# Kernel optimization log

Measured on AMD Instinct MI355X. Metric: run time of the kernel, lower is better.

The kernel has to match this reference:

```python
import jax, jax.numpy as jnp
import numpy as np

# ---- static config (mirrors CE defaults) ----
PS = 7        # patch size
WS = 27       # search window (per side)
S0 = 4        # query stride (stride0)
KS = 100      # k_s: top-k kept by search
KA = 100      # k_a: top-k used for aggregation
SCALE = 10.0  # softmax_scale
CI = 16       # inter_channels


def conv2d(x, w, b, pad):
    y = jax.lax.conv_general_dilated(
        x, w, (1, 1), [(pad, pad), (pad, pad)],
        dimension_numbers=("NCHW", "OIHW", "NCHW"))
    return y + b[None, :, None, None]


def all_patches(v):
    """[T,C,H,W] -> [T, H*W, C*PS*PS]; top-left anchored PSxPS patches,
    edge-clamped at the border (dnls-style bounded patch extraction)."""
    t, c, h, w = v.shape
    ii = jnp.clip(jnp.arange(h)[:, None] + jnp.arange(PS)[None, :], 0, h - 1)
    jj = jnp.clip(jnp.arange(w)[:, None] + jnp.arange(PS)[None, :], 0, w - 1)
    p = v[:, :, ii][:, :, :, :, jj]          # [T,C,H,PS,W,PS]
    p = p.transpose(0, 2, 4, 1, 3, 5)        # [T,H,W,C,PS,PS]
    return p.reshape(t, h * w, c * PS * PS)


def setup_inputs():
    key = jax.random.key(0)
    ks = jax.random.split(key, 4)
    vid = jax.random.normal(ks[0], (4, 64, 128, 128), jnp.float32)
    g_w = jax.random.normal(ks[1], (CI, 64, 3, 3), jnp.float32) * 0.05
    g_b = jnp.zeros((CI,), jnp.float32)
    theta_w = jax.random.normal(ks[2], (CI, 64, 1, 1), jnp.float32) * 0.1
    theta_b = jnp.zeros((CI,), jnp.float32)
    return {"vid": vid, "g_w": g_w, "g_b": g_b,
            "theta_w": theta_w, "theta_b": theta_b}


def reference(vid, g_w, g_b, theta_w, theta_b):
    t, c, h, w = vid.shape
    nH, nW = h // S0, w // S0
    Q, N = nH * nW, h * w

    # feature extraction (g -> search features, theta -> aggregation values)
    v1 = conv2d(vid, g_w, g_b, 1)          # [T,CI,H,W]
    v2 = conv2d(vid, theta_w, theta_b, 0)  # [T,CI,H,W]

    # windowed k-NN patch search: query grid (stride0) vs all keys (stride1=1)
    P1 = all_patches(v1)                                    # [T,N,D]
    qis = jnp.arange(nH) * S0
    qjs = jnp.arange(nW) * S0
    qflat = (qis[:, None] * w + qjs[None, :]).reshape(-1)   # [Q]
    Pq = P1[:, qflat]                                       # [T,Q,D]
    scores = jnp.einsum("tqd,tnd->tqn", Pq, P1)             # [T,Q,N]

    off = jnp.arange(WS) - WS // 2
    ci = jnp.clip(qis[:, None] + off, 0, h - 1)             # [nH,WS]
    cj = jnp.clip(qjs[:, None] + off, 0, w - 1)             # [nW,WS]
    cand = (ci[:, None, :, None] * w + cj[None, :, None, :]).reshape(Q, WS * WS)
    dists = jnp.take_along_axis(scores, cand[None], axis=2)  # [T,Q,WS*WS]

    d_k, widx = jax.lax.top_k(dists, KS)                    # [T,Q,KS]
    inds = jnp.take_along_axis(jnp.broadcast_to(cand[None], dists.shape),
                               widx, axis=2)                # flat key positions

    # top-k softmax aggregation weights
    wgt = jax.nn.softmax(d_k[..., :KA] * SCALE, axis=-1)    # [T,Q,KA]
    inds_a = inds[..., :KA]

    # wpsum: weighted sum of value patches gathered at neighbor indices,
    # expressed as sparse-scatter matrix @ dense patch matrix
    A = jnp.zeros((t, Q, N), scores.dtype).at[
        jnp.arange(t)[:, None, None],
        jnp.arange(Q)[None, :, None],
        inds_a].add(wgt)                                    # [T,Q,N]
    P2 = all_patches(v2)                                    # [T,N,D]
    z = jnp.einsum("tqn,tnd->tqd", A, P2)                   # [T,Q,CI*PS*PS]

    # ifold: scatter-add overlapping patches + count normalization
    z = z.reshape(t, Q, CI, PS, PS).transpose(0, 2, 1, 3, 4)
    z = z.reshape(t, CI, Q * PS * PS)
    ri = jnp.clip(qis[:, None] + jnp.arange(PS), 0, h - 1)  # [nH,PS]
    rj = jnp.clip(qjs[:, None] + jnp.arange(PS), 0, w - 1)  # [nW,PS]
    pix = (ri[:, None, :, None] * w + rj[None, :, None, :]).reshape(-1)
    Y = jnp.zeros((t, CI, N), z.dtype).at[:, :, pix].add(z)
    Zc = jnp.zeros((N,), z.dtype).at[pix].add(1.0)
    y = (Y / Zc).reshape(t, CI, h, w)
    return y
```

## Files before the change

kernel.cpp:

```cpp
#include <hip/hip_runtime.h>
#include <hip/hip_bf16.h>

#define T_ 4
#define C_ 64
#define H_ 128
#define W_ 128
#define CI_ 16
#define PS_ 7
#define NC_ 729
#define S0_ 4
#define KS_ 100
#define NQ_ 1024
#define SCALE_ 10.0f
#define HW_ (H_*W_)
#define RW_ 45
#define LCAP_ 768
#define CB_ 8

typedef float v2f __attribute__((ext_vector_type(2)));
#if __has_builtin(__builtin_elementwise_fma)
#define VFMA(a, b, c) __builtin_elementwise_fma((a), (b), (c))
#else
#define VFMA(a, b, c) ((a) * (b) + (c))
#endif

__device__ __forceinline__ float4 colfix(float4 r, bool loB, bool hiB) {
  float4 o;
  o.x = loB ? 0.f : (hiB ? r.y : r.x);
  o.y = loB ? r.x : (hiB ? r.z : r.y);
  o.z = loB ? r.y : (hiB ? r.w : r.z);
  o.w = loB ? r.z : (hiB ? 0.f : r.w);
  return o;
}

__global__ __launch_bounds__(128, 1) void conv3x3_kernel(
    const float* __restrict__ vid, const float* __restrict__ gw,
    const float* __restrict__ gb, float4* __restrict__ v1cs) {
  __shared__ float wls[C_ * 9 * 4];
  const int tid = threadIdx.x;
  const int g = blockIdx.y, t = blockIdx.z;
  for (int m = tid; m < C_ * 9 * 4; m += 128) {
    int co = m & 3, ck = m >> 2;
    wls[m] = gw[((size_t)(g * 4 + co) * C_) * 9 + ck];
  }
  __syncthreads();
  const int ti0 = (blockIdx.x >> 3) * 16, tj0 = (blockIdx.x & 7) * 16;
  const int u = tid >> 3, v = tid & 7;
  const int i = ti0 + u, j0 = tj0 + 2 * v;
  const int c0 = j0 - 1;
  const int c0c = min(max(c0, 0), W_ - 4);
  const bool loB = (c0 < 0), hiB = (c0 > W_ - 4);
  const int rm1 = max(i - 1, 0), rp1 = min(i + 1, H_ - 1);
  const float mk0 = (i > 0) ? 1.f : 0.f;
  const float mk2 = (i < H_ - 1) ? 1.f : 0.f;
  const int o0 = rm1 * W_ + c0c, o1 = i * W_ + c0c, o2 = rp1 * W_ + c0c;

  float accA[4], accB[4];
#pragma unroll
  for (int co = 0; co < 4; ++co) { accA[co] = gb[g * 4 + co]; accB[co] = gb[g * 4 + co]; }

  const float* vb = vid + ((size_t)t * C_) * HW_;
#pragma unroll 1
  for (int cb = 0; cb < C_; cb += CB_) {
    float4 r[CB_][3];
#pragma unroll
    for (int c = 0; c < CB_; ++c) {
      const float* p = vb + (size_t)(cb + c) * HW_;
      r[c][0] = *(const float4*)(p + o0);
      r[c][1] = *(const float4*)(p + o1);
      r[c][2] = *(const float4*)(p + o2);
    }
#pragma unroll
    for (int c = 0; c < CB_; ++c) {
      float4 f0 = colfix(r[c][0], loB, hiB);
      float4 f1 = colfix(r[c][1], loB, hiB);
      float4 f2 = colfix(r[c][2], loB, hiB);
      f0.x *= mk0; f0.y *= mk0; f0.z *= mk0; f0.w *= mk0;
      f2.x *= mk2; f2.y *= mk2; f2.z *= mk2; f2.w *= mk2;
      const float* wc = &wls[(cb + c) * 36];
      float e0[4] = {f0.x, f0.y, f0.z, f0.w};
      float e1[4] = {f1.x, f1.y, f1.z, f1.w};
      float e2[4] = {f2.x, f2.y, f2.z, f2.w};
#pragma unroll
      for (int kj = 0; kj < 3; ++kj) {
#pragma unroll
        for (int co = 0; co < 4; ++co) {
          accA[co] = fmaf(wc[(0 * 3 + kj) * 4 + co], e0[kj],     accA[co]);
          accB[co] = fmaf(wc[(0 * 3 + kj) * 4 + co], e0[kj + 1], accB[co]);
          accA[co] = fmaf(wc[(1 * 3 + kj) * 4 + co], e1[kj],     accA[co]);
          accB[co] = fmaf(wc[(1 * 3 + kj) * 4 + co], e1[kj + 1], accB[co]);
          accA[co] = fmaf(wc[(2 * 3 + kj) * 4 + co], e2[kj],     accA[co]);
          accB[co] = fmaf(wc[(2 * 3 + kj) * 4 + co], e2[kj + 1], accB[co]);
        }
      }
    }
  }
  const size_t o = ((size_t)g * T_ + t) * HW_ + i * W_ + j0;
  v1cs[o]     = make_float4(accA[0], accA[1], accA[2], accA[3]);
  v1cs[o + 1] = make_float4(accB[0], accB[1], accB[2], accB[3]);
}

__global__ __launch_bounds__(256, 1) void conv1x1_kernel(
    const float* __restrict__ vid, const float* __restrict__ tw,
    const float* __restrict__ tb, float4* __restrict__ v2cs) {
  __shared__ float w[C_ * 4];
  const int t = blockIdx.y, cc = blockIdx.z;
  for (int m = threadIdx.x; m < C_ * 4; m += 256) {
    int o = m & 3, c = m >> 2;
    w[m] = tw[(cc * 4 + o) * C_ + c];
  }
  __syncthreads();
  const int pix = blockIdx.x * 256 + threadIdx.x;
  float acc[4];
#pragma unroll
  for (int o = 0; o < 4; ++o) acc[o] = tb[cc * 4 + o];
  const float* vb = vid + ((size_t)t * C_) * HW_ + pix;
#pragma unroll 1
  for (int c0 = 0; c0 < C_; c0 += 16) {
    float x[16];
#pragma unroll
    for (int uu = 0; uu < 16; ++uu) x[uu] = vb[(size_t)(c0 + uu) * HW_];
#pragma unroll
    for (int uu = 0; uu < 16; ++uu)
#pragma unroll
      for (int o = 0; o < 4; ++o)
        acc[o] = fmaf(w[(c0 + uu) * 4 + o], x[uu], acc[o]);
  }
  v2cs[((size_t)cc * T_ + t) * HW_ + pix] = make_float4(acc[0], acc[1], acc[2], acc[3]);
}

__global__ __launch_bounds__(512, 2) void dist_kernel(
    const float4* __restrict__ v1cs, float* __restrict__ distG,
    float* __restrict__ distB, int nch) {
  __shared__ float4 Rs[2][2048];
  const int tid = threadIdx.x;
  const int t = blockIdx.y;
  const int half = blockIdx.z;
  const int cbase = half * 2;
  const int qi0 = (blockIdx.x >> 3) * 16, qj0 = (blockIdx.x & 7) * 16;
  const int w = tid >> 6, lane = tid & 63;
  const int pr = w >> 2, dj = (w & 3) * 4;
  const int rbase = 8 * pr;
  const int qi_p = qi0 + rbase;
  const int qj = qj0 + dj;
  const int la = lane >> 1, bg = lane & 1;
  const int b_lo = max(13 - qj, 0);
  const int bs = bg ? 13 : b_lo;
  const int a_lo0 = max(13 - qi_p, 0);
  const int a_lo1 = max(9 - qi_p, 0);
  const bool compute_ok = (la < 31);

  int soff[4];
#pragma unroll
  for (int k = 0; k < 4; ++k) {
    int p = min(tid + 512 * k, RW_ * RW_ - 1);
    int uu = p / RW_, vv = p - uu * RW_;
    int row = min(max(qi0 - 13 + uu, 0), H_ - 1);
    int col = min(max(qj0 - 13 + vv, 0), W_ - 1);
    soff[k] = row * W_ + col;
  }

  v2f acc0[14], acc1[14];
#pragma unroll
  for (int j = 0; j < 14; ++j) { acc0[j] = (v2f){0.f, 0.f}; acc1[j] = (v2f){0.f, 0.f}; }

  float4 st[4];
  {
    const float4* src = v1cs + ((size_t)cbase * T_ + t) * HW_;
#pragma unroll
    for (int k = 0; k < 4; ++k) st[k] = src[soff[k]];
  }
  int cur = 0;
#pragma unroll 1
  for (int ci = 0; ci < nch; ++ci) {
    float4* buf = &Rs[cur][0];
#pragma unroll
    for (int k = 0; k < 4; ++k) buf[tid + 512 * k] = st[k];
    if (ci + 1 < nch) {
      const float4* src = v1cs + ((size_t)(cbase + ci + 1) * T_ + t) * HW_;
#pragma unroll
      for (int k = 0; k < 4; ++k) st[k] = src[soff[k]];
    }
    __syncthreads();
    if (compute_ok) {
#pragma unroll 1
      for (int r = 0; r < 7; ++r) {
        v2f q0lo[7], q0hi[7], q1lo[7], q1hi[7];
        const float4* q0row = &buf[(rbase + 13 + r) * RW_ + dj + 13];
#pragma unroll
        for (int s = 0; s < 7; ++s) {
          float4 qq = q0row[s];
          q0lo[s] = (v2f){qq.x, qq.y};
          q0hi[s] = (v2f){qq.z, qq.w};
          float4 q2 = q0row[4 * RW_ + s];
          q1lo[s] = (v2f){q2.x, q2.y};
          q1hi[s] = (v2f){q2.z, q2.w};
        }
        const float4* crow = &buf[(rbase + la + r) * RW_ + dj + bs];
#pragma unroll
        for (int y = 0; y < 20; ++y) {
          float4 vv4 = crow[y];
          v2f vlo = (v2f){vv4.x, vv4.y}, vhi = (v2f){vv4.z, vv4.w};
          const int s_lo = (y > 13) ? (y - 13) : 0;
          const int s_hi = (y < 6) ? y : 6;
#pragma unroll
          for (int s = s_lo; s <= s_hi; ++s) {
            int j = y - s;
            acc0[j] = VFMA(q0lo[s], vlo, acc0[j]);
            acc0[j] = VFMA(q0hi[s], vhi, acc0[j]);
            acc1[j] = VFMA(q1lo[s], vlo, acc1[j]);
            acc1[j] = VFMA(q1hi[s], vhi, acc1[j]);
          }
        }
      }
    }
    cur ^= 1;
  }
  if (compute_ok) {
    float* outB = half ? distB : distG;
    const int q0q = ((qi_p >> 2) << 5) + (qj >> 2);
    if (la >= a_lo0 && la <= 26) {
      float* out = outB + ((size_t)t * NQ_ + q0q) * NC_ + la * 27 + bs;
#pragma unroll
      for (int j = 0; j < 14; ++j) out[j] = acc0[j].x + acc0[j].y;
    }
    const int a1 = la - 4;
    if (a1 >= a_lo1 && a1 <= 26) {
      float* out = outB + ((size_t)t * NQ_ + (q0q + 32)) * NC_ + a1 * 27 + bs;
#pragma unroll
      for (int j = 0; j < 14; ++j) out[j] = acc1[j].x + acc1[j].y;
    }
  }
}

__global__ __launch_bounds__(256) void select_kernel(
    const float* __restrict__ distA, const float* __restrict__ distB, int dual,
    int* __restrict__ sel_n, float* __restrict__ sel_w,
    float* __restrict__ wsum_out) {
  __shared__ float dist[NC_];
  __shared__ unsigned int ukey[NC_];
  __shared__ float redf[4];
  __shared__ unsigned int hist[256];
  __shared__ int lk[LCAP_];
  __shared__ unsigned int lkey[LCAP_];
  __shared__ unsigned int scal[6];

  const int tid = threadIdx.x;
  const int lane = tid & 63, wid = tid >> 6;
  const int q = blockIdx.x, t = blockIdx.y;
  const int qi = (q >> 5) * S0_, qj = (q & 31) * S0_;
  const int a_lo = max(13 - qi, 0), b_lo = max(13 - qj, 0);
  const size_t base = ((size_t)t * NQ_ + q) * NC_;

  for (int h = tid; h < 256; h += 256) hist[h] = 0;
  if (tid == 0) { scal[2] = 0; scal[3] = 0; }
  float lmax = -INFINITY;
  for (int k = tid; k < NC_; k += 256) {
    int aa = k / 27, bb = k - aa * 27;
    int kk = max(aa, a_lo) * 27 + max(bb, b_lo);
    float d = distA[base + kk];
    if (dual) d += distB[base + kk];
    dist[k] = d;
    unsigned int u = __float_as_uint(d);
    ukey[k] = u ^ (((unsigned int)((int)u >> 31)) | 0x80000000u);
    lmax = fmaxf(lmax, d);
  }
#pragma unroll
  for (int off = 32; off > 0; off >>= 1)
    lmax = fmaxf(lmax, __shfl_down(lmax, off, 64));
  if (lane == 0) redf[wid] = lmax;
  __syncthreads();
  const float dmax = fmaxf(fmaxf(redf[0], redf[1]), fmaxf(redf[2], redf[3]));
  for (int k = tid; k < NC_; k += 256) atomicAdd(&hist[ukey[k] >> 24], 1u);
  __syncthreads();
  if (wid == 0) {
    int s4 = (int)(hist[lane * 4] + hist[lane * 4 + 1] + hist[lane * 4 + 2] + hist[lane * 4 + 3]);
    int s = s4;
#pragma unroll
    for (int off = 1; off < 64; off <<= 1) {
      int o = __shfl_down(s, off, 64);
      if (lane + off < 64) s += o;
    }
    int above = s - s4;
    if (above < KS_ && s >= KS_) {
      int run = above;
#pragma unroll
      for (int bb = 3; bb >= 0; --bb) {
        int h = (int)hist[lane * 4 + bb];
        if (run + h >= KS_) { scal[0] = (unsigned int)(lane * 4 + bb); scal[1] = (unsigned int)run; break; }
        run += h;
      }
    }
  }
  __syncthreads();
  const unsigned int beta = scal[0];
  const int run = (int)scal[1];
  for (int h = tid; h < 256; h += 256) hist[h] = 0;
  __syncthreads();
  for (int k = tid; k < NC_; k += 256)
    if ((ukey[k] >> 24) == beta) atomicAdd(&hist[(ukey[k] >> 16) & 0xFFu], 1u);
  __syncthreads();
  if (wid == 0) {
    int s4 = (int)(hist[lane * 4] + hist[lane * 4 + 1] + hist[lane * 4 + 2] + hist[lane * 4 + 3]);
    int s = s4;
#pragma unroll
    for (int off = 1; off < 64; off <<= 1) {
      int o = __shfl_down(s, off, 64);
      if (lane + off < 64) s += o;
    }
    int above = run + s - s4;
    if (above < KS_ && run + s >= KS_) {
      int r2 = above;
#pragma unroll
      for (int bb = 3; bb >= 0; --bb) {
        int h = (int)hist[lane * 4 + bb];
        if (r2 + h >= KS_) { scal[4] = (unsigned int)(lane * 4 + bb); scal[5] = (unsigned int)r2; break; }
        r2 += h;
      }
    }
  }
  __syncthreads();
  const unsigned int beta2 = scal[4];
  const int run2 = (int)scal[5];
  const size_t outb = ((size_t)t * NQ_ + q) * KS_;
  float lsum = 0.f;
  for (int k = tid; k < NC_; k += 256) {
    unsigned int key = ukey[k];
    unsigned int bin = key >> 24;
    bool sel = false, bdry = false;
    if (bin > beta) sel = true;
    else if (bin == beta) {
      unsigned int b2 = (key >> 16) & 0xFFu;
      if (b2 > beta2) sel = true;
      else if (b2 == beta2) bdry = true;
    }
    if (sel) {
      unsigned int slot = atomicAdd(&scal[2], 1u);
      int aa = k / 27, bb = k - aa * 27;
      int ni = min(max(qi + aa - 13, 0), H_ - 1);
      int nj = min(max(qj + bb - 13, 0), W_ - 1);
      float wv = __expf(SCALE_ * (dist[k] - dmax));
      sel_n[outb + slot] = (ni << 7) | nj;
      sel_w[outb + slot] = wv;
      lsum += wv;
    } else if (bdry) {
      unsigned int pos = atomicAdd(&scal[3], 1u);
      if (pos < LCAP_) { lk[pos] = k; lkey[pos] = key; }
    }
  }
  __syncthreads();
  const int L = min((int)scal[3], LCAP_);
  for (int i = tid; i < L; i += 256) {
    unsigned int key = lkey[i];
    int k = lk[i];
    int cnt = run2;
    for (int m = 0; m < L; ++m)
      cnt += (int)((lkey[m] > key) || (lkey[m] == key && lk[m] < k));
    if (cnt < KS_) {
      unsigned int slot = atomicAdd(&scal[2], 1u);
      int aa = k / 27, bb = k - aa * 27;
      int ni = min(max(qi + aa - 13, 0), H_ - 1);
      int nj = min(max(qj + bb - 13, 0), W_ - 1);
      float wv = __expf(SCALE_ * (dist[k] - dmax));
      sel_n[outb + slot] = (ni << 7) | nj;
      sel_w[outb + slot] = wv;
      lsum += wv;
    }
  }
#pragma unroll
  for (int off = 32; off > 0; off >>= 1) lsum += __shfl_down(lsum, off, 64);
  __syncthreads();
  if (lane == 0) redf[wid] = lsum;
  __syncthreads();
  if (tid == 0) wsum_out[t * NQ_ + q] = (redf[0] + redf[1]) + (redf[2] + redf[3]);
}

__global__ __launch_bounds__(1024) void agg_kernel(
    const float4* __restrict__ v2cs, const int* __restrict__ sel_n,
    const float* __restrict__ sel_w, const float* __restrict__ wsum,
    float* __restrict__ Y) {
  __shared__ float4 Rs[RW_ * RW_];
  __shared__ int s_off[16][KS_];
  __shared__ float s_w[16][KS_];
  const int tid = threadIdx.x;
  const int t = blockIdx.y;
  const int qi0 = (blockIdx.x >> 3) * 16, qj0 = (blockIdx.x & 7) * 16;
  const int w = tid >> 6, lane = tid & 63;
  const int di = (w >> 2) * 4, dj = (w & 3) * 4;
  const int qi = qi0 + di, qj = qj0 + dj;
  const int q = ((qi >> 2) << 5) + (qj >> 2);
  const size_t base = ((size_t)t * NQ_ + q) * KS_;
  const float inv = 1.0f / wsum[t * NQ_ + q];
  for (int k = lane; k < KS_; k += 64) {
    int n = sel_n[base + k];
    int ni = n >> 7, nj = n & 127;
    s_off[w][k] = (ni - qi0 + 13) * RW_ + (nj - qj0 + 13);
    s_w[w][k] = sel_w[base + k] * inv;
  }
  const int r = lane / 7, s = lane - r * 7;
  const int myo = r * RW_ + s;
  const int oi = min(qi + r, H_ - 1), oj = min(qj + s, W_ - 1);
#pragma unroll 1
  for (int cc = 0; cc < 4; ++cc) {
    __syncthreads();
    const float4* src = v2cs + ((size_t)cc * T_ + t) * HW_;
    for (int p = tid; p < RW_ * RW_; p += 1024) {
      int uu = p / RW_, vv = p - uu * RW_;
      int row = min(max(qi0 - 13 + uu, 0), H_ - 1);
      int col = min(max(qj0 - 13 + vv, 0), W_ - 1);
      Rs[p] = src[row * W_ + col];
    }
    __syncthreads();
    if (lane < 49) {
      float4 acc = make_float4(0.f, 0.f, 0.f, 0.f);
#pragma unroll 4
      for (int k = 0; k < KS_; ++k) {
        float wv = s_w[w][k];
        float4 v = Rs[s_off[w][k] + myo];
        acc.x = fmaf(wv, v.x, acc.x);
        acc.y = fmaf(wv, v.y, acc.y);
        acc.z = fmaf(wv, v.z, acc.z);
        acc.w = fmaf(wv, v.w, acc.w);
      }
      float* yb = Y + (((size_t)t * CI_ + cc * 4) * H_ + oi) * W_ + oj;
      atomicAdd(yb, acc.x);
      atomicAdd(yb + HW_, acc.y);
      atomicAdd(yb + 2 * HW_, acc.z);
      atomicAdd(yb + 3 * HW_, acc.w);
    }
  }
}

__device__ __forceinline__ int cov_axis(int x) {
  int c = 0;
#pragma unroll
  for (int r = 0; r < 7; ++r) {
    if (x < H_ - 1) {
      int qb = x - r;
      c += (qb >= 0 && (qb & 3) == 0) ? 1 : 0;
    } else {
      c += (r >= 3) ? 1 : 0;
    }
  }
  return c;
}

__global__ void norm_kernel(float* __restrict__ Y) {
  int idx = blockIdx.x * blockDim.x + threadIdx.x;
  if (idx >= T_ * CI_ * HW_) return;
  int p = idx & (HW_ - 1);
  float z = (float)(cov_axis(p >> 7) * cov_axis(p & 127));
  Y[idx] /= z;
}

extern "C" void kernel_launch(void* const* d_in, const int* in_sizes, int n_in,
                              void* d_out, int out_size, void* d_ws, size_t ws_size,
                              hipStream_t stream) {
  const float* vid     = (const float*)d_in[0];
  const float* g_w     = (const float*)d_in[1];
  const float* g_b     = (const float*)d_in[2];
  const float* theta_w = (const float*)d_in[3];
  const float* theta_b = (const float*)d_in[4];
  float* Y = (float*)d_out;

  float* v1cs  = (float*)d_ws;
  float* v2cs  = v1cs + (size_t)4 * T_ * HW_ * 4;
  float* distG = v2cs + (size_t)4 * T_ * HW_ * 4;
  int*   sel_n = (int*)(distG + (size_t)T_ * NQ_ * NC_);
  float* sel_w = (float*)(sel_n + (size_t)T_ * NQ_ * KS_);
  float* wsumv = sel_w + (size_t)T_ * NQ_ * KS_;
  float* distB = wsumv + (size_t)T_ * NQ_;

  const size_t need_dual =
      ((size_t)4 * T_ * HW_ * 4 * 2 + (size_t)T_ * NQ_ * NC_ * 2 +
       (size_t)T_ * NQ_ * KS_ * 2 + (size_t)T_ * NQ_) * sizeof(float);
  const int dual = (ws_size >= need_dual) ? 1 : 0;

  hipMemsetAsync(Y, 0, (size_t)out_size * sizeof(float), stream);

  conv3x3_kernel<<<dim3(64, 4, T_), 128, 0, stream>>>(vid, g_w, g_b, (float4*)v1cs);
  conv1x1_kernel<<<dim3(HW_ / 256, T_, 4), 256, 0, stream>>>(vid, theta_w, theta_b, (float4*)v2cs);
  dist_kernel<<<dim3(64, T_, dual ? 2 : 1), 512, 0, stream>>>(
      (const float4*)v1cs, distG, distB, dual ? 2 : 4);
  select_kernel<<<dim3(NQ_, T_), 256, 0, stream>>>(distG, distB, dual, sel_n, sel_w, wsumv);
  agg_kernel<<<dim3(64, T_), 1024, 0, stream>>>((const float4*)v2cs, sel_n, sel_w, wsumv, Y);
  norm_kernel<<<(T_ * CI_ * HW_ + 255) / 256, 256, 0, stream>>>(Y);
}
```

Measured before the change: 266.6 us.

## Split dist kernel work by patch rows instead of channel halves, sharing loaded tiles

The distance kernel previously split the four feature-channel groups across two grid z-slices, each loading its own halo tiles. Now one 1024-thread block loads all four channel groups once, and two 8-wave sets each compute a subset of patch rows (0-3 and 4-6) into separate partial buffers. The select kernel sums these partials as before. A fallback path uses atomics into a zeroed buffer when workspace is small. This halves global tile loads and grid size but adds an extra barrier per channel and an uneven row split (4 vs 3) between the wave sets.

```diff
diff --git a/kernel.cpp b/kernel.cpp
--- a/kernel.cpp
+++ b/kernel.cpp
@@ -129,17 +129,17 @@
   v2cs[((size_t)cc * T_ + t) * HW_ + pix] = make_float4(acc[0], acc[1], acc[2], acc[3]);
 }
 
-__global__ __launch_bounds__(512, 2) void dist_kernel(
+__global__ __launch_bounds__(1024, 4) void dist_kernel(
     const float4* __restrict__ v1cs, float* __restrict__ distG,
-    float* __restrict__ distB, int nch) {
-  __shared__ float4 Rs[2][2048];
+    float* __restrict__ distB, int use_atomic) {
+  __shared__ float4 Rs[2][2025];
   const int tid = threadIdx.x;
   const int t = blockIdx.y;
-  const int half = blockIdx.z;
-  const int cbase = half * 2;
   const int qi0 = (blockIdx.x >> 3) * 16, qj0 = (blockIdx.x & 7) * 16;
   const int w = tid >> 6, lane = tid & 63;
-  const int pr = w >> 2, dj = (w & 3) * 4;
+  const int ws = w & 7, rset = w >> 3;
+  const int r0 = rset ? 4 : 0, r1 = rset ? 7 : 4;
+  const int pr = ws >> 2, dj = (ws & 3) * 4;
   const int rbase = 8 * pr;
   const int qi_p = qi0 + rbase;
   const int qj = qj0 + dj;
@@ -149,42 +149,44 @@
   const int a_lo0 = max(13 - qi_p, 0);
   const int a_lo1 = max(9 - qi_p, 0);
   const bool compute_ok = (la < 31);
-
-  int soff[4];
-#pragma unroll
-  for (int k = 0; k < 4; ++k) {
-    int p = min(tid + 512 * k, RW_ * RW_ - 1);
+  const bool bdup = (bg == 0) && (b_lo == 13);
+
+  int soff[2];
+#pragma unroll
+  for (int k = 0; k < 2; ++k) {
+    int p = min(tid + 1024 * k, RW_ * RW_ - 1);
     int uu = p / RW_, vv = p - uu * RW_;
     int row = min(max(qi0 - 13 + uu, 0), H_ - 1);
     int col = min(max(qj0 - 13 + vv, 0), W_ - 1);
     soff[k] = row * W_ + col;
   }
+  const int d0 = tid, d1 = min(tid + 1024, RW_ * RW_ - 1);
 
   v2f acc0[14], acc1[14];
 #pragma unroll
   for (int j = 0; j < 14; ++j) { acc0[j] = (v2f){0.f, 0.f}; acc1[j] = (v2f){0.f, 0.f}; }
 
-  float4 st[4];
+  float4 st[2];
   {
-    const float4* src = v1cs + ((size_t)cbase * T_ + t) * HW_;
-#pragma unroll
-    for (int k = 0; k < 4; ++k) st[k] = src[soff[k]];
+    const float4* src = v1cs + ((size_t)0 * T_ + t) * HW_;
+    st[0] = src[soff[0]];
+    st[1] = src[soff[1]];
   }
   int cur = 0;
 #pragma unroll 1
-  for (int ci = 0; ci < nch; ++ci) {
+  for (int ci = 0; ci < 4; ++ci) {
     float4* buf = &Rs[cur][0];
-#pragma unroll
-    for (int k = 0; k < 4; ++k) buf[tid + 512 * k] = st[k];
-    if (ci + 1 < nch) {
-      const float4* src = v1cs + ((size_t)(cbase + ci + 1) * T_ + t) * HW_;
-#pragma unroll
-      for (int k = 0; k < 4; ++k) st[k] = src[soff[k]];
+    buf[d0] = st[0];
+    buf[d1] = st[1];
+    if (ci < 3) {
+      const float4* src = v1cs + ((size_t)(ci + 1) * T_ + t) * HW_;
+      st[0] = src[soff[0]];
+      st[1] = src[soff[1]];
     }
     __syncthreads();
     if (compute_ok) {
 #pragma unroll 1
-      for (int r = 0; r < 7; ++r) {
+      for (int r = r0; r < r1; ++r) {
         v2f q0lo[7], q0hi[7], q1lo[7], q1hi[7];
         const float4* q0row = &buf[(rbase + 13 + r) * RW_ + dj + 13];
 #pragma unroll
@@ -214,21 +216,32 @@
         }
       }
     }
+    __syncthreads();
     cur ^= 1;
   }
   if (compute_ok) {
-    float* outB = half ? distB : distG;
+    float* outB = (rset && !use_atomic) ? distB : distG;
     const int q0q = ((qi_p >> 2) << 5) + (qj >> 2);
-    if (la >= a_lo0 && la <= 26) {
+    if (la >= a_lo0 && la <= 26 && !(use_atomic && bdup)) {
       float* out = outB + ((size_t)t * NQ_ + q0q) * NC_ + la * 27 + bs;
-#pragma unroll
-      for (int j = 0; j < 14; ++j) out[j] = acc0[j].x + acc0[j].y;
+      if (use_atomic) {
+#pragma unroll
+        for (int j = 0; j < 14; ++j) atomicAdd(out + j, acc0[j].x + acc0[j].y);
+      } else {
+#pragma unroll
+        for (int j = 0; j < 14; ++j) out[j] = acc0[j].x + acc0[j].y;
+      }
     }
     const int a1 = la - 4;
-    if (a1 >= a_lo1 && a1 <= 26) {
+    if (a1 >= a_lo1 && a1 <= 26 && !(use_atomic && bdup)) {
       float* out = outB + ((size_t)t * NQ_ + (q0q + 32)) * NC_ + a1 * 27 + bs;
-#pragma unroll
-      for (int j = 0; j < 14; ++j) out[j] = acc1[j].x + acc1[j].y;
+      if (use_atomic) {
+#pragma unroll
+        for (int j = 0; j < 14; ++j) atomicAdd(out + j, acc1[j].x + acc1[j].y);
+      } else {
+#pragma unroll
+        for (int j = 0; j < 14; ++j) out[j] = acc1[j].x + acc1[j].y;
+      }
     }
   }
 }
@@ -477,11 +490,13 @@
   const int dual = (ws_size >= need_dual) ? 1 : 0;
 
   hipMemsetAsync(Y, 0, (size_t)out_size * sizeof(float), stream);
+  if (!dual)
+    hipMemsetAsync(distG, 0, (size_t)T_ * NQ_ * NC_ * sizeof(float), stream);
 
   conv3x3_kernel<<<dim3(64, 4, T_), 128, 0, stream>>>(vid, g_w, g_b, (float4*)v1cs);
   conv1x1_kernel<<<dim3(HW_ / 256, T_, 4), 256, 0, stream>>>(vid, theta_w, theta_b, (float4*)v2cs);
-  dist_kernel<<<dim3(64, T_, dual ? 2 : 1), 512, 0, stream>>>(
-      (const float4*)v1cs, distG, distB, dual ? 2 : 4);
+  dist_kernel<<<dim3(64, T_), 1024, 0, stream>>>(
+      (const float4*)v1cs, distG, distB, dual ? 0 : 1);
   select_kernel<<<dim3(NQ_, T_), 256, 0, stream>>>(distG, distB, dual, sel_n, sel_w, wsumv);
   agg_kernel<<<dim3(64, T_), 1024, 0, stream>>>((const float4*)v2cs, sel_n, sel_w, wsumv, Y);
   norm_kernel<<<(T_ * CI_ * HW_ + 255) / 256, 256, 0, stream>>>(Y);
```

New measurement: 364.6 us. 36.8% more time.
